# Kernel optimization log

Measured on AMD Instinct MI355X. Metric: run time of the kernel, lower is better.

## Reference

```python
import jax, jax.numpy as jnp
import numpy as np

B, N, D = 32, 540, 512
H = 8
DH = D // H
MAX_LEN = 540
POS_CLIP = MAX_LEN - 1


def setup_inputs() -> dict:
    key = jax.random.key(0)
    ks = jax.random.split(key, 12)
    s = 0.02
    inp = {
        "query": jax.random.normal(ks[0], (B, N, D), dtype=jnp.float32),
        "Wq": jax.random.normal(ks[1], (D, D), dtype=jnp.float32) * s,
        "bq": jnp.zeros((D,), jnp.float32),
        "Wk": jax.random.normal(ks[2], (D, D), dtype=jnp.float32) * s,
        "bk": jnp.zeros((D,), jnp.float32),
        "Wv": jax.random.normal(ks[3], (D, D), dtype=jnp.float32) * s,
        "bv": jnp.zeros((D,), jnp.float32),
        "Wh": jax.random.normal(ks[4], (D, D), dtype=jnp.float32) * s,
        "bh": jnp.zeros((D,), jnp.float32),
        "pos_k": jax.random.uniform(ks[5], (2 * POS_CLIP + 1, DH), dtype=jnp.float32, minval=-0.05, maxval=0.05),
        "gamma": jnp.ones((D,), jnp.float32),
        "beta": jnp.zeros((D,), jnp.float32),
        "valid_len": jax.random.randint(ks[6], (B,), 1, N + 1, dtype=jnp.int32),
    }
    return inp


def _split_heads(x):
    # [B, N, D] -> [H*B, N, DH], head-major on axis 0 (matches tf.concat(tf.split(x,H,-1),0))
    return x.reshape(B, N, H, DH).transpose(2, 0, 1, 3).reshape(H * B, N, DH)


def reference(query, Wq, bq, Wk, bk, Wv, bv, Wh, bh, pos_k, gamma, beta, valid_len):
    q = _split_heads(query @ Wq + bq)  # [HB, N, DH]
    k = _split_heads(query @ Wk + bk)
    v = _split_heads(query @ Wv + bv)

    QK = jnp.einsum("xqd,xkd->xqk", q, k)  # [HB, N, N]

    # relative position bias (Shaw et al. 2018)
    rel = jnp.arange(N)[None, :] - jnp.arange(N)[:, None]
    rel = jnp.clip(rel, -POS_CLIP, POS_CLIP) + POS_CLIP
    pos_enc_k = pos_k[rel]  # [N, N, DH]
    QR = jnp.einsum("xqd,qkd->xqk", q, pos_enc_k)

    attn = (QK + QR) / jnp.sqrt(jnp.float32(DH))

    # key-side sequence mask, broadcast over heads and query rows
    key_mask = jnp.arange(N)[None, :] < valid_len[:, None]  # [B, N]
    key_mask = jnp.tile(key_mask[:, None, :], (H, N, 1))  # [HB, N, N]
    attn = jnp.where(key_mask, attn, jnp.float32(-1e12))
    attn = jax.nn.softmax(attn, axis=-1)

    out = jnp.einsum("xqk,xkd->xqd", attn, v)  # [HB, N, DH]
    out = out.reshape(H, B, N, DH).transpose(1, 2, 0, 3).reshape(B, N, D)
    out = out @ Wh + bh
    out = out + query

    # layer norm over last axis
    mean = jnp.mean(out, axis=-1, keepdims=True)
    var = jnp.mean(jnp.square(out - mean), axis=-1, keepdims=True)
    normalized = (out - mean) * jax.lax.rsqrt(var + 1e-7)
    return gamma * normalized + beta
```

## Files before the change

### kernel.cpp

```cpp
#include <hip/hip_runtime.h>
#include <hip/hip_bf16.h>

typedef __hip_bfloat16 bf16;

#define NB 32
#define NSEQ 540
#define ND 512
#define NH 8
#define NDH 64
#define NHB 256
#define NM 17280
#define NPOS 1079
#define VTP 544

typedef __bf16 v8bf __attribute__((ext_vector_type(8)));
typedef float f32x4 __attribute__((ext_vector_type(4)));

union U8 {
  uint4 u;
  unsigned short s[8];
  v8bf v;
};

union U2 {
  uint2 u;
  unsigned short s[4];
};

__device__ __forceinline__ unsigned short f2b(float x) {
  union { float f; unsigned u; } c;
  c.f = x;
  const unsigned r = c.u + 0x7fffu + ((c.u >> 16) & 1u);
  return (unsigned short)(r >> 16);
}

__device__ __forceinline__ float b2f16(unsigned short s) {
  return __uint_as_float(((unsigned)s) << 16);
}

__device__ __forceinline__ void bar_lds() {
  asm volatile("s_waitcnt lgkmcnt(0)\n\ts_barrier" ::: "memory");
}

__device__ __forceinline__ int xcd_swz(int p, int total) {
  const int g = p >> 5, r = p & 31;
  return ((g << 5) + 32 <= total) ? ((g << 5) + ((r & 7) << 2) + (r >> 3)) : p;
}

__device__ __forceinline__ void gl_lds16(const unsigned short* g,
                                         unsigned short* l) {
  __builtin_amdgcn_global_load_lds(
      (const __attribute__((address_space(1))) unsigned int*)g,
      (__attribute__((address_space(3))) unsigned int*)l, 16, 0, 0);
}

__device__ __forceinline__ void cvt16(const float* __restrict__ p,
                                      unsigned short* __restrict__ dst) {
  unsigned short s[16];
#pragma unroll
  for (int i = 0; i < 4; i++) {
    const float4 v = *(const float4*)(p + i * 4);
    s[i * 4 + 0] = f2b(v.x);
    s[i * 4 + 1] = f2b(v.y);
    s[i * 4 + 2] = f2b(v.z);
    s[i * 4 + 3] = f2b(v.w);
  }
  *(uint4*)dst = *(uint4*)s;
  *(uint4*)(dst + 8) = *(uint4*)(s + 8);
}

__global__ __launch_bounds__(256) void prep(
    const float* __restrict__ x, unsigned short* __restrict__ xb,
    const float* __restrict__ pos, unsigned short* __restrict__ posb,
    const float* __restrict__ Wq, const float* __restrict__ Wk,
    const float* __restrict__ Wv, const float* __restrict__ Wh,
    unsigned short* __restrict__ Wt) {
  __shared__ unsigned short T[64][72];
  const int blk = blockIdx.x;
  const int tid = threadIdx.x;
  if (blk < 4320) {
    const int i = blk * 256 + tid;
    const float4 a = *(const float4*)(x + (size_t)i * 8);
    const float4 b = *(const float4*)(x + (size_t)i * 8 + 4);
    unsigned short s[8];
    s[0] = f2b(a.x); s[1] = f2b(a.y); s[2] = f2b(a.z); s[3] = f2b(a.w);
    s[4] = f2b(b.x); s[5] = f2b(b.y); s[6] = f2b(b.z); s[7] = f2b(b.w);
    *(uint4*)(xb + (size_t)i * 8) = *(uint4*)s;
  } else if (blk < 4590) {
    const int i = (blk - 4320) * 256 + tid;
    if (i < NPOS * NDH) posb[i] = f2b(pos[i]);
  } else {
    const int idx = blk - 4590;
    const int sel = idx >> 6;
    const int rem = idx & 63;
    const float* W = (sel == 0) ? Wq : (sel == 1) ? Wk : (sel == 2) ? Wv : Wh;
    unsigned short* out = Wt + (size_t)sel * ND * ND;
    const int k0 = (rem & 7) * 64, n0 = (rem >> 3) * 64;
    const int r = tid >> 2, g = tid & 3;
    cvt16(W + (size_t)(k0 + r) * ND + n0 + g * 16, &T[r][g * 16]);
    __syncthreads();
    unsigned short s[16];
#pragma unroll
    for (int j = 0; j < 16; j++) s[j] = T[g * 16 + j][r];
    unsigned short* dst = out + (size_t)(n0 + r) * ND + k0 + g * 16;
    *(uint4*)dst = *(uint4*)s;
    *(uint4*)(dst + 8) = *(uint4*)(s + 8);
  }
}

#define GEMM_CORE_B16(APTR)                                                       \
  {                                                                               \
    const int lrow = lane >> 2;                                                   \
    const int lc8 = (lane & 3) * 8;                                               \
    const int arow = 32 * w + lrow;                   \
    unsigned short* lA0 = &As[0][0] + (size_t)(2 * w) * 512;                      \
    unsigned short* lB0 = &Bs[0][0] + (size_t)(2 * w) * 512;                      \
    for (int k0 = 0; k0 < 512; k0 += 32) {                                        \
      __syncthreads();                                                            \
      gl_lds16(APTR + (size_t)(m0 + arow) * ND + k0 + lc8, lA0);                  \
      gl_lds16(APTR + (size_t)(m0 + arow + 16) * ND + k0 + lc8, lA0 + 512);       \
      gl_lds16(Bt + (size_t)(n0 + arow) * ND + k0 + lc8, lB0);                    \
      gl_lds16(Bt + (size_t)(n0 + arow + 16) * ND + k0 + lc8, lB0 + 512);         \
      __syncthreads();                                                            \
      U8 af[4], bfr[4];                                                           \
      _Pragma("unroll")                                                           \
      for (int mi = 0; mi < 4; mi++)                                              \
        af[mi].u = *(const uint4*)&As[wr * 64 + mi * 16 + l15][quad * 8];         \
      _Pragma("unroll")                                                           \
      for (int ni = 0; ni < 4; ni++)                                              \
        bfr[ni].u = *(const uint4*)&Bs[wc * 64 + ni * 16 + l15][quad * 8];        \
      _Pragma("unroll")                                                           \
      for (int mi = 0; mi < 4; mi++)                                              \
        _Pragma("unroll")                                                         \
        for (int ni = 0; ni < 4; ni++)                                            \
          acc[mi][ni] = __builtin_amdgcn_mfma_f32_16x16x32_bf16(                  \
              af[mi].v, bfr[ni].v, acc[mi][ni], 0, 0, 0);                         \
    }                                                                             \
  }

__global__ __launch_bounds__(256, 3) void qkv_mfma(
    const unsigned short* __restrict__ Xb, const unsigned short* __restrict__ Wt,
    const float* __restrict__ bq, const float* __restrict__ bk,
    const float* __restrict__ bv, const int* __restrict__ vlen,
    bf16* __restrict__ qh, bf16* __restrict__ kh, bf16* __restrict__ vt) {
  __shared__ unsigned short As[128][32];
  __shared__ unsigned short Bs[128][32];
  const int tid = threadIdx.x;
  const int phys = blockIdx.x + (blockIdx.y << 2) + 540 * blockIdx.z;
  const int W = xcd_swz(phys, 1620);
  const int sel = W / 540;
  const int rem = W - sel * 540;
  const int m0 = (rem >> 2) * 128, n0 = (rem & 3) * 128;

  if (sel != 0) {
    const int gran = (sel == 1) ? 63 : 31;
    const int b0 = m0 / NSEQ;
    const int b1 = (m0 + 127) / NSEQ;
    bool needed = false;
    for (int bb = b0; bb <= b1; ++bb) {
      const int s_lo = (bb == b0) ? (m0 - b0 * NSEQ) : 0;
      const int thr = (vlen[bb] + gran) & ~gran;
      if (s_lo < thr) needed = true;
    }
    if (!needed) return;
  }

  const unsigned short* Bt = Wt + (size_t)sel * ND * ND;
  const float* bias = (sel == 0) ? bq : (sel == 1) ? bk : bv;
  const int lane = tid & 63, w = tid >> 6;
  const int wr = w & 1, wc = w >> 1;
  const int l15 = lane & 15, quad = lane >> 4;

  f32x4 acc[4][4];
#pragma unroll
  for (int mi = 0; mi < 4; mi++)
#pragma unroll
    for (int ni = 0; ni < 4; ni++) acc[mi][ni] = (f32x4){0.f, 0.f, 0.f, 0.f};

  GEMM_CORE_B16(Xb)

  if (sel != 2) {
    unsigned short* o = (unsigned short*)((sel == 0) ? qh : kh);
#pragma unroll
    for (int mi = 0; mi < 4; mi++) {
      const int m = m0 + wr * 64 + mi * 16 + quad * 4;
      const int bidx = m / NSEQ;
      const int seq0 = m - bidx * NSEQ;
#pragma unroll
      for (int ni = 0; ni < 4; ni++) {
        const int n = n0 + wc * 64 + ni * 16 + l15;
        const int h = n >> 6, dh = n & 63;
        const float bsv = bias[n];
        const size_t base = (((size_t)(h * NB + bidx)) * NSEQ + seq0) * NDH + dh;
#pragma unroll
        for (int i = 0; i < 4; i++)
          o[base + (size_t)i * NDH] = f2b(acc[mi][ni][i] + bsv);
      }
    }
  } else {
    unsigned short* o = (unsigned short*)vt;
#pragma unroll
    for (int mi = 0; mi < 4; mi++) {
      const int m = m0 + wr * 64 + mi * 16 + quad * 4;
      const int bidx = m / NSEQ;
      const int seq0 = m - bidx * NSEQ;
#pragma unroll
      for (int ni = 0; ni < 4; ni++) {
        const int n = n0 + wc * 64 + ni * 16 + l15;
        const int h = n >> 6, dh = n & 63;
        const float bsv = bias[n];
        unsigned short pk[4];
#pragma unroll
        for (int i = 0; i < 4; i++) pk[i] = f2b(acc[mi][ni][i] + bsv);
        *(uint2*)(o + (((size_t)(h * NB + bidx)) * NDH + dh) * VTP + seq0) =
            *(uint2*)pk;
      }
    }
  }
}

__global__ __launch_bounds__(256, 3) void out_mfma(
    const unsigned short* __restrict__ ctxb, const unsigned short* __restrict__ Wht,
    const float* __restrict__ bh, const float* __restrict__ query,
    float* __restrict__ tmp) {
  __shared__ unsigned short As[128][32];
  __shared__ unsigned short Bs[128][32];
  const int tid = threadIdx.x;
  const unsigned short* Bt = Wht;
  const int phys = blockIdx.x + (blockIdx.y << 2);
  const int W = xcd_swz(phys, 540);
  const int m0 = (W >> 2) * 128, n0 = (W & 3) * 128;
  const int lane = tid & 63, w = tid >> 6;
  const int wr = w & 1, wc = w >> 1;
  const int l15 = lane & 15, quad = lane >> 4;

  f32x4 acc[4][4];
#pragma unroll
  for (int mi = 0; mi < 4; mi++)
#pragma unroll
    for (int ni = 0; ni < 4; ni++) acc[mi][ni] = (f32x4){0.f, 0.f, 0.f, 0.f};

  GEMM_CORE_B16(ctxb)

#pragma unroll
  for (int mi = 0; mi < 4; mi++) {
    const int m = m0 + wr * 64 + mi * 16 + quad * 4;
#pragma unroll
    for (int ni = 0; ni < 4; ni++) {
      const int n = n0 + wc * 64 + ni * 16 + l15;
      const float bsv = bh[n];
#pragma unroll
      for (int i = 0; i < 4; i++) {
        const size_t off = (size_t)(m + i) * ND + n;
        tmp[off] = acc[mi][ni][i] + bsv + query[off];
      }
    }
  }
}

#define PW 584

__global__ __launch_bounds__(256, 6) void attn(
    const bf16* __restrict__ qh, const bf16* __restrict__ kh,
    const bf16* __restrict__ vt, const unsigned short* __restrict__ posb,
    const int* __restrict__ vlen, bf16* __restrict__ ctx) {
  __shared__ unsigned short P[16][PW];
  __shared__ float Tt[16][84];
  __shared__ float red4[16][4];
  __shared__ float sinv[16];

  const int tid = threadIdx.x;
  const int lane = tid & 63;
  const int w = tid >> 6;
  const int l15 = lane & 15;
  const int quad = lane >> 4;
  const int qb = blockIdx.x;
  const int x = blockIdx.y;
  const int b = x & 31, h = x >> 5;
  const int q0 = qb * 16;
  const int valid = vlen[b];
  const int NT = (valid + 63) >> 6;
  const int NC = (valid + 31) >> 5;
  const bf16* qbase = qh + (size_t)x * NSEQ * NDH;
  const unsigned short* kbase = (const unsigned short*)(kh + (size_t)x * NSEQ * NDH);
  const unsigned short* vbase = (const unsigned short*)(vt + (size_t)x * NDH * VTP);

  U8 aq0, aq1;
  {
    const int q = q0 + l15;
    if (q < NSEQ) {
      aq0.u = *(const uint4*)(qbase + (size_t)q * NDH + quad * 8);
      aq1.u = *(const uint4*)(qbase + (size_t)q * NDH + 32 + quad * 8);
    } else {
      aq0.u = make_uint4(0, 0, 0, 0);
      aq1.u = make_uint4(0, 0, 0, 0);
    }
  }

  U8 ck0, ck1, cp0, cp1, ce0, ce1;
  {
    const int key = w * 16 + l15;
    ck0.u = *(const uint4*)(kbase + (size_t)key * NDH + quad * 8);
    ck1.u = *(const uint4*)(kbase + (size_t)key * NDH + 32 + quad * 8);
    const long pr = (long)(524 - q0 + w * 16 + l15);
    cp0.u = *(const uint4*)(posb + pr * NDH + quad * 8);
    cp1.u = *(const uint4*)(posb + pr * NDH + 32 + quad * 8);
    if (w == 0) {
      const long pr2 = (long)(524 - q0 + 64 + l15);
      ce0.u = *(const uint4*)(posb + pr2 * NDH + quad * 8);
      ce1.u = *(const uint4*)(posb + pr2 * NDH + 32 + quad * 8);
    }
  }

  float sl = 0.f;

  for (int kt = 0; kt < NT; kt++) {
    U8 nk0, nk1, np0, np1, ne0, ne1;
    if (kt < NT - 1) {
      const int k1 = kt * 64 + 64;
      const int key = k1 + w * 16 + l15;
      nk0.u = *(const uint4*)(kbase + (size_t)key * NDH + quad * 8);
      nk1.u = *(const uint4*)(kbase + (size_t)key * NDH + 32 + quad * 8);
      const long pr = (long)(k1 - q0 + 524 + w * 16 + l15);
      np0.u = *(const uint4*)(posb + pr * NDH + quad * 8);
      np1.u = *(const uint4*)(posb + pr * NDH + 32 + quad * 8);
      if (w == 0) {
        const long pr2 = (long)(k1 - q0 + 524 + 64 + l15);
        ne0.u = *(const uint4*)(posb + pr2 * NDH + quad * 8);
        ne1.u = *(const uint4*)(posb + pr2 * NDH + 32 + quad * 8);
      }
    }

    f32x4 accqk = {0.f, 0.f, 0.f, 0.f};
    accqk = __builtin_amdgcn_mfma_f32_16x16x32_bf16(ck0.v, aq0.v, accqk, 0, 0, 0);
    accqk = __builtin_amdgcn_mfma_f32_16x16x32_bf16(ck1.v, aq1.v, accqk, 0, 0, 0);
    f32x4 accT = {0.f, 0.f, 0.f, 0.f};
    accT = __builtin_amdgcn_mfma_f32_16x16x32_bf16(cp0.v, aq0.v, accT, 0, 0, 0);
    accT = __builtin_amdgcn_mfma_f32_16x16x32_bf16(cp1.v, aq1.v, accT, 0, 0, 0);
    f32x4 accT2 = {0.f, 0.f, 0.f, 0.f};
    if (w == 0) {
      accT2 = __builtin_amdgcn_mfma_f32_16x16x32_bf16(ce0.v, aq0.v, accT2, 0, 0, 0);
      accT2 = __builtin_amdgcn_mfma_f32_16x16x32_bf16(ce1.v, aq1.v, accT2, 0, 0, 0);
    }

    bar_lds();
    *(f32x4*)&Tt[l15][w * 16 + quad * 4] = accT;
    if (w == 0) *(f32x4*)&Tt[l15][64 + quad * 4] = accT2;
    bar_lds();
    {
      const int k0 = kt * 64;
      const int cb = w * 16 + quad * 4;
      const int jb = cb + 15 - l15;
      U2 pk;
#pragma unroll
      for (int i = 0; i < 4; i++) {
        const float v = (accqk[i] + Tt[l15][jb + i]) * 0.125f;
        const float e = ((k0 + cb + i) < valid) ? __expf(v) : 0.f;
        pk.s[i] = f2b(e);
        sl += e;
      }
      *(uint2*)&P[l15][k0 + cb] = pk.u;
    }
    ck0 = nk0; ck1 = nk1; cp0 = np0; cp1 = np1;
    if (w == 0) { ce0 = ne0; ce1 = ne1; }
  }

  sl += __shfl_xor(sl, 16, 64);
  sl += __shfl_xor(sl, 32, 64);
  if (quad == 0) red4[l15][w] = sl;

  {
    const int r = tid >> 4, c = tid & 15;
    const int ch0 = NT * 8;
    for (int ch = c; ch < 72; ch += 16) {
      if (ch >= ch0) *(uint4*)&P[r][ch * 8] = make_uint4(0, 0, 0, 0);
    }
  }

  const int dh = w * 16 + l15;
  const unsigned short* vrow = vbase + (size_t)dh * VTP;
  U8 cv;
  cv.u = *(const uint4*)(vrow + quad * 8);

  bar_lds();

  if (tid < 16) {
    const float4 rs = *(const float4*)red4[tid];
    sinv[tid] = 1.f / (rs.x + rs.y + rs.z + rs.w);
  }
  bar_lds();

  f32x4 acco = {0.f, 0.f, 0.f, 0.f};
  for (int ci = 0; ci < NC; ci++) {
    U8 nv_;
    if (ci + 1 < NC) nv_.u = *(const uint4*)(vrow + (ci + 1) * 32 + quad * 8);
    U8 ap;
    ap.u = *(const uint4*)&P[l15][ci * 32 + quad * 8];
    acco = __builtin_amdgcn_mfma_f32_16x16x32_bf16(ap.v, cv.v, acco, 0, 0, 0);
    cv = nv_;
  }
  unsigned short* ob = (unsigned short*)ctx;
#pragma unroll
  for (int i = 0; i < 4; i++) {
    const int q = q0 + quad * 4 + i;
    if (q < NSEQ) {
      ob[((size_t)b * NSEQ + q) * ND + h * NDH + dh] =
          f2b(acco[i] * sinv[quad * 4 + i]);
    }
  }
}

__global__ __launch_bounds__(256) void lnorm(
    const float* __restrict__ tmp, const float* __restrict__ gamma,
    const float* __restrict__ beta, float* __restrict__ out) {
  const int w = threadIdx.x >> 6, lane = threadIdx.x & 63;
  const int row = blockIdx.x * 4 + w;
  const size_t base = (size_t)row * 512 + lane * 8;
  const float4 a = *(const float4*)(tmp + base);
  const float4 b = *(const float4*)(tmp + base + 4);

  float s = a.x + a.y + a.z + a.w + b.x + b.y + b.z + b.w;
#pragma unroll
  for (int m = 1; m < 64; m <<= 1) s += __shfl_xor(s, m, 64);
  const float mean = s * (1.f / 512.f);

  float d[8] = {a.x - mean, a.y - mean, a.z - mean, a.w - mean,
                b.x - mean, b.y - mean, b.z - mean, b.w - mean};
  float v = 0.f;
#pragma unroll
  for (int i = 0; i < 8; i++) v += d[i] * d[i];
#pragma unroll
  for (int m = 1; m < 64; m <<= 1) v += __shfl_xor(v, m, 64);
  const float rstd = rsqrtf(v * (1.f / 512.f) + 1e-7f);

  const int col = lane * 8;
  const float4 g0 = *(const float4*)(gamma + col);
  const float4 g1 = *(const float4*)(gamma + col + 4);
  const float4 be0 = *(const float4*)(beta + col);
  const float4 be1 = *(const float4*)(beta + col + 4);
  float4 o0, o1;
  o0.x = d[0] * rstd * g0.x + be0.x;
  o0.y = d[1] * rstd * g0.y + be0.y;
  o0.z = d[2] * rstd * g0.z + be0.z;
  o0.w = d[3] * rstd * g0.w + be0.w;
  o1.x = d[4] * rstd * g1.x + be1.x;
  o1.y = d[5] * rstd * g1.y + be1.y;
  o1.z = d[6] * rstd * g1.z + be1.z;
  o1.w = d[7] * rstd * g1.w + be1.w;
  *(float4*)(out + base) = o0;
  *(float4*)(out + base + 4) = o1;
}

extern "C" void kernel_launch(void* const* d_in, const int* in_sizes, int n_in,
                              void* d_out, int out_size, void* d_ws, size_t ws_size,
                              hipStream_t stream) {
  const float* query = (const float*)d_in[0];
  const float* Wq = (const float*)d_in[1];
  const float* bq = (const float*)d_in[2];
  const float* Wk = (const float*)d_in[3];
  const float* bk = (const float*)d_in[4];
  const float* Wv = (const float*)d_in[5];
  const float* bv = (const float*)d_in[6];
  const float* Wh = (const float*)d_in[7];
  const float* bh = (const float*)d_in[8];
  const float* pos = (const float*)d_in[9];
  const float* gamma = (const float*)d_in[10];
  const float* beta = (const float*)d_in[11];
  const int* vlen = (const int*)d_in[12];

  bf16* ws = (bf16*)d_ws;
  const size_t QSZ = (size_t)NHB * NSEQ * NDH;
  const size_t VSZ = (size_t)NHB * NDH * VTP;
  bf16* qh = ws;
  bf16* kh = ws + QSZ;
  bf16* vt = ws + 2 * QSZ;
  unsigned short* posb = (unsigned short*)(ws + 2 * QSZ + VSZ);
  unsigned short* Wtb = posb + (size_t)NPOS * NDH;
  unsigned short* Xb = (unsigned short*)d_out;
  bf16* ctx = (bf16*)d_out;
  float* tmp = (float*)d_ws;
  (void)ws_size;

  prep<<<dim3(4846), 256, 0, stream>>>(query, Xb, pos, posb, Wq, Wk, Wv, Wh, Wtb);
  qkv_mfma<<<dim3(4, 135, 3), 256, 0, stream>>>(Xb, Wtb, bq, bk, bv, vlen, qh, kh, vt);
  attn<<<dim3(34, 256), 256, 0, stream>>>(qh, kh, vt, posb, vlen, ctx);
  out_mfma<<<dim3(4, 135), 256, 0, stream>>>((const unsigned short*)ctx,
                                             Wtb + 3 * (size_t)ND * ND, bh, query, tmp);
  lnorm<<<dim3(4320), 256, 0, stream>>>(tmp, gamma, beta, (float*)d_out);
}
```

Measured before the change: 293.9 us.

## Process 128 keys per attention score iteration with doubled prefetch

The attention score loop now handles two 64-key groups per iteration, with double-buffered K and positional operands. This halves the number of barrier/LDS round trips, and the positional scratch buffer is widened to match. K projection skipping is coarsened to 128-key granularity so the extra keys exist. Launch bounds are lowered from 6 to 4 waves per SIMD to accommodate the extra registers, at the risk of lower occupancy and out-of-range positional/K reads on the tail tiles.

```diff
diff --git a/kernel.cpp b/kernel.cpp
--- a/kernel.cpp
+++ b/kernel.cpp
@@ -153,7 +153,7 @@
   const int m0 = (rem >> 2) * 128, n0 = (rem & 3) * 128;
 
   if (sel != 0) {
-    const int gran = (sel == 1) ? 63 : 31;
+    const int gran = (sel == 1) ? 127 : 31;
     const int b0 = m0 / NSEQ;
     const int b1 = (m0 + 127) / NSEQ;
     bool needed = false;
@@ -208,7 +208,7 @@
       for (int ni = 0; ni < 4; ni++) {
         const int n = n0 + wc * 64 + ni * 16 + l15;
         const int h = n >> 6, dh = n & 63;
-        const float bsv = bias[n];
+        const float bsv = bv[n];
         unsigned short pk[4];
 #pragma unroll
         for (int i = 0; i < 4; i++) pk[i] = f2b(acc[mi][ni][i] + bsv);
@@ -260,12 +260,12 @@
 
 #define PW 584
 
-__global__ __launch_bounds__(256, 6) void attn(
+__global__ __launch_bounds__(256, 4) void attn(
     const bf16* __restrict__ qh, const bf16* __restrict__ kh,
     const bf16* __restrict__ vt, const unsigned short* __restrict__ posb,
     const int* __restrict__ vlen, bf16* __restrict__ ctx) {
   __shared__ unsigned short P[16][PW];
-  __shared__ float Tt[16][84];
+  __shared__ float Tt[16][148];
   __shared__ float red4[16][4];
   __shared__ float sinv[16];
 
@@ -279,7 +279,7 @@
   const int b = x & 31, h = x >> 5;
   const int q0 = qb * 16;
   const int valid = vlen[b];
-  const int NT = (valid + 63) >> 6;
+  const int NT2 = (valid + 127) >> 7;
   const int NC = (valid + 31) >> 5;
   const bf16* qbase = qh + (size_t)x * NSEQ * NDH;
   const unsigned short* kbase = (const unsigned short*)(kh + (size_t)x * NSEQ * NDH);
@@ -297,72 +297,97 @@
     }
   }
 
-  U8 ck0, ck1, cp0, cp1, ce0, ce1;
+  U8 kA0, kA1, kB0, kB1, pA0, pA1, pB0, pB1, pC0, pC1;
   {
-    const int key = w * 16 + l15;
-    ck0.u = *(const uint4*)(kbase + (size_t)key * NDH + quad * 8);
-    ck1.u = *(const uint4*)(kbase + (size_t)key * NDH + 32 + quad * 8);
+    const int keyA = w * 16 + l15;
+    kA0.u = *(const uint4*)(kbase + (size_t)keyA * NDH + quad * 8);
+    kA1.u = *(const uint4*)(kbase + (size_t)keyA * NDH + 32 + quad * 8);
+    kB0.u = *(const uint4*)(kbase + (size_t)(keyA + 64) * NDH + quad * 8);
+    kB1.u = *(const uint4*)(kbase + (size_t)(keyA + 64) * NDH + 32 + quad * 8);
     const long pr = (long)(524 - q0 + w * 16 + l15);
-    cp0.u = *(const uint4*)(posb + pr * NDH + quad * 8);
-    cp1.u = *(const uint4*)(posb + pr * NDH + 32 + quad * 8);
+    pA0.u = *(const uint4*)(posb + pr * NDH + quad * 8);
+    pA1.u = *(const uint4*)(posb + pr * NDH + 32 + quad * 8);
+    pB0.u = *(const uint4*)(posb + (pr + 64) * NDH + quad * 8);
+    pB1.u = *(const uint4*)(posb + (pr + 64) * NDH + 32 + quad * 8);
     if (w == 0) {
-      const long pr2 = (long)(524 - q0 + 64 + l15);
-      ce0.u = *(const uint4*)(posb + pr2 * NDH + quad * 8);
-      ce1.u = *(const uint4*)(posb + pr2 * NDH + 32 + quad * 8);
+      const long pr2 = (long)(524 - q0 + 128 + l15);
+      pC0.u = *(const uint4*)(posb + pr2 * NDH + quad * 8);
+      pC1.u = *(const uint4*)(posb + pr2 * NDH + 32 + quad * 8);
     }
   }
 
   float sl = 0.f;
 
-  for (int kt = 0; kt < NT; kt++) {
-    U8 nk0, nk1, np0, np1, ne0, ne1;
-    if (kt < NT - 1) {
-      const int k1 = kt * 64 + 64;
-      const int key = k1 + w * 16 + l15;
-      nk0.u = *(const uint4*)(kbase + (size_t)key * NDH + quad * 8);
-      nk1.u = *(const uint4*)(kbase + (size_t)key * NDH + 32 + quad * 8);
+  for (int kt = 0; kt < NT2; kt++) {
+    U8 nkA0, nkA1, nkB0, nkB1, npA0, npA1, npB0, npB1, npC0, npC1;
+    if (kt < NT2 - 1) {
+      const int k1 = kt * 128 + 128;
+      const int keyA = k1 + w * 16 + l15;
+      nkA0.u = *(const uint4*)(kbase + (size_t)keyA * NDH + quad * 8);
+      nkA1.u = *(const uint4*)(kbase + (size_t)keyA * NDH + 32 + quad * 8);
+      nkB0.u = *(const uint4*)(kbase + (size_t)(keyA + 64) * NDH + quad * 8);
+      nkB1.u = *(const uint4*)(kbase + (size_t)(keyA + 64) * NDH + 32 + quad * 8);
       const long pr = (long)(k1 - q0 + 524 + w * 16 + l15);
-      np0.u = *(const uint4*)(posb + pr * NDH + quad * 8);
-      np1.u = *(const uint4*)(posb + pr * NDH + 32 + quad * 8);
+      npA0.u = *(const uint4*)(posb + pr * NDH + quad * 8);
+      npA1.u = *(const uint4*)(posb + pr * NDH + 32 + quad * 8);
+      npB0.u = *(const uint4*)(posb + (pr + 64) * NDH + quad * 8);
+      npB1.u = *(const uint4*)(posb + (pr + 64) * NDH + 32 + quad * 8);
       if (w == 0) {
-        const long pr2 = (long)(k1 - q0 + 524 + 64 + l15);
-        ne0.u = *(const uint4*)(posb + pr2 * NDH + quad * 8);
-        ne1.u = *(const uint4*)(posb + pr2 * NDH + 32 + quad * 8);
+        const long pr2 = (long)(k1 - q0 + 524 + 128 + l15);
+        npC0.u = *(const uint4*)(posb + pr2 * NDH + quad * 8);
+        npC1.u = *(const uint4*)(posb + pr2 * NDH + 32 + quad * 8);
       }
     }
 
-    f32x4 accqk = {0.f, 0.f, 0.f, 0.f};
-    accqk = __builtin_amdgcn_mfma_f32_16x16x32_bf16(ck0.v, aq0.v, accqk, 0, 0, 0);
-    accqk = __builtin_amdgcn_mfma_f32_16x16x32_bf16(ck1.v, aq1.v, accqk, 0, 0, 0);
-    f32x4 accT = {0.f, 0.f, 0.f, 0.f};
-    accT = __builtin_amdgcn_mfma_f32_16x16x32_bf16(cp0.v, aq0.v, accT, 0, 0, 0);
-    accT = __builtin_amdgcn_mfma_f32_16x16x32_bf16(cp1.v, aq1.v, accT, 0, 0, 0);
-    f32x4 accT2 = {0.f, 0.f, 0.f, 0.f};
+    f32x4 aA = {0.f, 0.f, 0.f, 0.f};
+    aA = __builtin_amdgcn_mfma_f32_16x16x32_bf16(kA0.v, aq0.v, aA, 0, 0, 0);
+    aA = __builtin_amdgcn_mfma_f32_16x16x32_bf16(kA1.v, aq1.v, aA, 0, 0, 0);
+    f32x4 aB = {0.f, 0.f, 0.f, 0.f};
+    aB = __builtin_amdgcn_mfma_f32_16x16x32_bf16(kB0.v, aq0.v, aB, 0, 0, 0);
+    aB = __builtin_amdgcn_mfma_f32_16x16x32_bf16(kB1.v, aq1.v, aB, 0, 0, 0);
+    f32x4 tA = {0.f, 0.f, 0.f, 0.f};
+    tA = __builtin_amdgcn_mfma_f32_16x16x32_bf16(pA0.v, aq0.v, tA, 0, 0, 0);
+    tA = __builtin_amdgcn_mfma_f32_16x16x32_bf16(pA1.v, aq1.v, tA, 0, 0, 0);
+    f32x4 tB = {0.f, 0.f, 0.f, 0.f};
+    tB = __builtin_amdgcn_mfma_f32_16x16x32_bf16(pB0.v, aq0.v, tB, 0, 0, 0);
+    tB = __builtin_amdgcn_mfma_f32_16x16x32_bf16(pB1.v, aq1.v, tB, 0, 0, 0);
+    f32x4 tC = {0.f, 0.f, 0.f, 0.f};
     if (w == 0) {
-      accT2 = __builtin_amdgcn_mfma_f32_16x16x32_bf16(ce0.v, aq0.v, accT2, 0, 0, 0);
-      accT2 = __builtin_amdgcn_mfma_f32_16x16x32_bf16(ce1.v, aq1.v, accT2, 0, 0, 0);
+      tC = __builtin_amdgcn_mfma_f32_16x16x32_bf16(pC0.v, aq0.v, tC, 0, 0, 0);
+      tC = __builtin_amdgcn_mfma_f32_16x16x32_bf16(pC1.v, aq1.v, tC, 0, 0, 0);
     }
 
     bar_lds();
-    *(f32x4*)&Tt[l15][w * 16 + quad * 4] = accT;
-    if (w == 0) *(f32x4*)&Tt[l15][64 + quad * 4] = accT2;
+    *(f32x4*)&Tt[l15][w * 16 + quad * 4] = tA;
+    *(f32x4*)&Tt[l15][64 + w * 16 + quad * 4] = tB;
+    if (w == 0) *(f32x4*)&Tt[l15][128 + quad * 4] = tC;
     bar_lds();
     {
-      const int k0 = kt * 64;
+      const int k0 = kt * 128;
       const int cb = w * 16 + quad * 4;
       const int jb = cb + 15 - l15;
       U2 pk;
 #pragma unroll
       for (int i = 0; i < 4; i++) {
-        const float v = (accqk[i] + Tt[l15][jb + i]) * 0.125f;
+        const float v = (aA[i] + Tt[l15][jb + i]) * 0.125f;
         const float e = ((k0 + cb + i) < valid) ? __expf(v) : 0.f;
         pk.s[i] = f2b(e);
         sl += e;
       }
       *(uint2*)&P[l15][k0 + cb] = pk.u;
-    }
-    ck0 = nk0; ck1 = nk1; cp0 = np0; cp1 = np1;
-    if (w == 0) { ce0 = ne0; ce1 = ne1; }
+      U2 pk2;
+#pragma unroll
+      for (int i = 0; i < 4; i++) {
+        const float v = (aB[i] + Tt[l15][jb + 64 + i]) * 0.125f;
+        const float e = ((k0 + 64 + cb + i) < valid) ? __expf(v) : 0.f;
+        pk2.s[i] = f2b(e);
+        sl += e;
+      }
+      *(uint2*)&P[l15][k0 + 64 + cb] = pk2.u;
+    }
+    kA0 = nkA0; kA1 = nkA1; kB0 = nkB0; kB1 = nkB1;
+    pA0 = npA0; pA1 = npA1; pB0 = npB0; pB1 = npB1;
+    if (w == 0) { pC0 = npC0; pC1 = npC1; }
   }
 
   sl += __shfl_xor(sl, 16, 64);
@@ -371,7 +396,7 @@
 
   {
     const int r = tid >> 4, c = tid & 15;
-    const int ch0 = NT * 8;
+    const int ch0 = NT2 * 16;
     for (int ch = c; ch < 72; ch += 16) {
       if (ch >= ch0) *(uint4*)&P[r][ch * 8] = make_uint4(0, 0, 0, 0);
     }
```

Measured after the change: 304.9 us. +3.8%, slower.
